# Performance work log

Hardware: AMD Instinct MI355X
Metric: run time of the kernel (lower is better)

The kernel has to match this reference:

```python
import jax, jax.numpy as jnp
import numpy as np

B, BARS, BEATS, FRAC = 64, 16, 4, 8
IN_F = 10 * 47 * 2  # 940
LIN_OUT = 100
BEAT_H = 16
BAR_H = 32


def _p(key, shape, scale=0.05):
    return jax.random.normal(key, shape, dtype=jnp.float32) * scale


def setup_inputs() -> dict:
    key = jax.random.key(0)
    ks = jax.random.split(key, 16)
    return {
        "channels": jax.random.normal(ks[0], (B, BARS, BEATS, FRAC, 10, 2, 47), dtype=jnp.float32),
        "lin_w": _p(ks[1], (LIN_OUT, IN_F)),
        "lin_b": _p(ks[2], (LIN_OUT,)),
        # beats LSTM (unidirectional), PyTorch gate order i,f,g,o
        "b_wih": _p(ks[3], (4 * BEAT_H, LIN_OUT)),
        "b_whh": _p(ks[4], (4 * BEAT_H, BEAT_H)),
        "b_bih": _p(ks[5], (4 * BEAT_H,)),
        "b_bhh": _p(ks[6], (4 * BEAT_H,)),
        # bars LSTM, bidirectional: forward (f_) and reverse (r_) directions
        "f_wih": _p(ks[7], (4 * BAR_H, BEAT_H)),
        "f_whh": _p(ks[8], (4 * BAR_H, BAR_H)),
        "f_bih": _p(ks[9], (4 * BAR_H,)),
        "f_bhh": _p(ks[10], (4 * BAR_H,)),
        "r_wih": _p(ks[11], (4 * BAR_H, BEAT_H)),
        "r_whh": _p(ks[12], (4 * BAR_H, BAR_H)),
        "r_bih": _p(ks[13], (4 * BAR_H,)),
        "r_bhh": _p(ks[14], (4 * BAR_H,)),
    }


def lstm(x, wih, whh, bih, bhh):
    """PyTorch-semantics LSTM, batch_first. x: [N, T, F] -> h_seq [N, T, H]."""
    N = x.shape[0]
    H = whh.shape[1]
    # precompute input contribution for all timesteps
    xg = jnp.einsum('ntf,gf->ntg', x, wih) + (bih + bhh)  # [N, T, 4H]

    def step(carry, xt):
        h, c = carry
        gates = xt + h @ whh.T  # [N, 4H]
        i, f, g, o = jnp.split(gates, 4, axis=-1)
        c = jax.nn.sigmoid(f) * c + jax.nn.sigmoid(i) * jnp.tanh(g)
        h = jax.nn.sigmoid(o) * jnp.tanh(c)
        return (h, c), h

    h0 = jnp.zeros((N, H), x.dtype)
    _, hs = jax.lax.scan(step, (h0, h0), jnp.swapaxes(xg, 0, 1))  # [T, N, H]
    return jnp.swapaxes(hs, 0, 1)


def bilstm(x, f_wih, f_whh, f_bih, f_bhh, r_wih, r_whh, r_bih, r_bhh):
    fwd = lstm(x, f_wih, f_whh, f_bih, f_bhh)
    bwd = jnp.flip(lstm(jnp.flip(x, axis=1), r_wih, r_whh, r_bih, r_bhh), axis=1)
    return jnp.concatenate([fwd, bwd], axis=-1)


def reference(channels, lin_w, lin_b,
              b_wih, b_whh, b_bih, b_bhh,
              f_wih, f_whh, f_bih, f_bhh,
              r_wih, r_whh, r_bih, r_bhh):
    # channels: [B, bars, beats, frac, 10, 2, 47]
    x = jnp.swapaxes(channels, -1, -2)  # [..., 10, 47, 2]
    x = x.reshape(*x.shape[:4], IN_F)   # squash dims 4..6 -> 940
    x = jax.nn.relu(x @ lin_w.T + lin_b)  # [B, bars, beats, frac, 100]

    # Distributed depth=2: fold (B, bars, beats) into batch, seq over frac
    xb = x.reshape(B * BARS * BEATS, FRAC, LIN_OUT)
    beats = lstm(xb, b_wih, b_whh, b_bih, b_bhh)
    beats = beats.reshape(B, BARS, BEATS, FRAC, BEAT_H)

    # last fraction hidden state, then Distributed depth=1 over beats axis
    xl = beats[:, :, :, -1].reshape(B * BARS, BEATS, BEAT_H)
    bars = bilstm(xl, f_wih, f_whh, f_bih, f_bhh, r_wih, r_whh, r_bih, r_bhh)
    bars = bars.reshape(B, BARS, BEATS, 2 * BAR_H)
    return beats, bars
```

## Files before the change

kernel.cpp:

```cpp
#include <hip/hip_runtime.h>
#include <hip/hip_bf16.h>

typedef float f32x4 __attribute__((ext_vector_type(4)));
typedef short bf16x8 __attribute__((ext_vector_type(8)));

#define MFMA16(a, b, c) __builtin_amdgcn_mfma_f32_16x16x32_bf16(a, b, c, 0, 0, 0)

constexpr int K1  = 940;
constexpr int KP2 = 1024;
constexpr int NP  = 112;
constexpr int OSL = 136;

__device__ __forceinline__ float sigf(float x) { return 1.f / (1.f + __expf(-x)); }
__device__ __forceinline__ float tanhfast(float x) { return 2.f / (1.f + __expf(-2.f * x)) - 1.f; }

__device__ __forceinline__ short f2b(float x) {
  __hip_bfloat16 b = __float2bfloat16(x);
  return *reinterpret_cast<short*>(&b);
}

__global__ void prep_kernel(const float* __restrict__ lin_w,
                            const float* __restrict__ b_wih,
                            __hip_bfloat16* __restrict__ w2,
                            __hip_bfloat16* __restrict__ bw2) {
  int idx = blockIdx.x * 256 + threadIdx.x;
  if (idx < NP * KP2) {
    int n = idx >> 10, k = idx & 1023;
    float v = 0.f;
    if (n < 100 && k < K1) {
      int c10 = k / 94, rem = k - c10 * 94;
      int c2 = rem / 47, c47 = rem - c2 * 47;
      int f = c10 * 94 + c47 * 2 + c2;
      v = lin_w[n * K1 + f];
    }
    w2[idx] = __float2bfloat16(v);
  } else {
    int i2 = idx - NP * KP2;
    if (i2 < 64 * 128) {
      int g = i2 >> 7, k = i2 & 127;
      bw2[i2] = __float2bfloat16((k < 100) ? b_wih[g * 100 + k] : 0.f);
    }
  }
}

__global__ __launch_bounds__(256, 2)
void fused_encoder(const float* __restrict__ ch,
                   const __hip_bfloat16* __restrict__ w2,
                   const float* __restrict__ lin_b,
                   const __hip_bfloat16* __restrict__ bw2,
                   const float* __restrict__ bih,
                   const float* __restrict__ bhh,
                   const float* __restrict__ whh,
                   float* __restrict__ beats) {
  __shared__ __align__(16) __hip_bfloat16 out_s[64 * OSL];
  __shared__ float xg_s[64 * 65];

  const int tid = threadIdx.x;
  const int w = tid >> 6, lane = tid & 63;
  const int l16 = lane & 15, bq = lane >> 4;

  const int mbase = blockIdx.x * 64 + w * 16;
  const float* ar = ch + (long)(mbase + l16) * K1 + bq * 8;

  int bidx[7];
#pragma unroll
  for (int nt = 0; nt < 7; ++nt) bidx[nt] = (nt * 16 + l16) * KP2 + bq * 8;

  float lb[7];
#pragma unroll
  for (int nt = 0; nt < 7; ++nt) {
    int col = nt * 16 + l16;
    lb[nt] = (col < 100) ? lin_b[col] : 0.f;
  }

  auto mk = [&](float4 lo, float4 hi) -> bf16x8 {
    return bf16x8{f2b(lo.x), f2b(lo.y), f2b(lo.z), f2b(lo.w),
                  f2b(hi.x), f2b(hi.y), f2b(hi.z), f2b(hi.w)};
  };

  f32x4 acc[7] = {};
  float4 Ab[2][4];
  bf16x8 Bb[2][7];

  const float4 f40{0.f, 0.f, 0.f, 0.f};
  auto ldA = [&](int c, float4* d) {
    const float* p = ar + c * 64;
    if (c < 14) {
      d[0] = *reinterpret_cast<const float4*>(p);
      d[1] = *reinterpret_cast<const float4*>(p + 4);
      d[2] = *reinterpret_cast<const float4*>(p + 32);
      d[3] = *reinterpret_cast<const float4*>(p + 36);
    } else {
      d[0] = *reinterpret_cast<const float4*>(p);
      d[1] = *reinterpret_cast<const float4*>(p + 4);
      d[2] = (bq <= 1) ? *reinterpret_cast<const float4*>(p + 32) : f40;
      d[3] = (bq == 0) ? *reinterpret_cast<const float4*>(p + 36) : f40;
    }
  };
  auto ldB = [&](int ks, bf16x8* d) {
#pragma unroll
    for (int nt = 0; nt < 7; ++nt)
      d[nt] = *reinterpret_cast<const bf16x8*>(&w2[bidx[nt] + ks * 32]);
  };

  ldA(0, Ab[0]);
  ldB(0, Bb[0]);
  ldB(1, Bb[1]);
#pragma unroll
  for (int c = 0; c < 15; ++c) {
    float4* A = Ab[c & 1];
    if (c < 14) ldA(c + 1, Ab[(c + 1) & 1]);
    {
      bf16x8 a = mk(A[0], A[1]);
#pragma unroll
      for (int nt = 0; nt < 7; ++nt) acc[nt] = MFMA16(a, Bb[0][nt], acc[nt]);
    }
    if (c < 14) ldB(2 * c + 2, Bb[0]);
    {
      bf16x8 a = mk(A[2], A[3]);
#pragma unroll
      for (int nt = 0; nt < 7; ++nt) acc[nt] = MFMA16(a, Bb[1][nt], acc[nt]);
    }
    if (c < 14) ldB(2 * c + 3, Bb[1]);
  }

#pragma unroll
  for (int nt = 0; nt < 7; ++nt) {
    const int col = nt * 16 + l16;
#pragma unroll
    for (int r = 0; r < 4; ++r) {
      float v = fmaxf(acc[nt][r] + lb[nt], 0.f);
      out_s[(w * 16 + bq * 4 + r) * OSL + col] = __float2bfloat16((col < 100) ? v : 0.f);
    }
  }
#pragma unroll
  for (int r = 0; r < 4; ++r)
    out_s[(w * 16 + bq * 4 + r) * OSL + 112 + l16] = __float2bfloat16(0.f);

  {
    bf16x8 av[4];
#pragma unroll
    for (int s = 0; s < 4; ++s)
      av[s] = *reinterpret_cast<const bf16x8*>(&out_s[(w * 16 + l16) * OSL + s * 32 + bq * 8]);
    f32x4 xacc[4] = {};
#pragma unroll
    for (int gt = 0; gt < 4; ++gt) {
#pragma unroll
      for (int s = 0; s < 4; ++s) {
        bf16x8 b = *reinterpret_cast<const bf16x8*>(&bw2[(gt * 16 + l16) * 128 + s * 32 + bq * 8]);
        xacc[gt] = MFMA16(av[s], b, xacc[gt]);
      }
    }
#pragma unroll
    for (int gt = 0; gt < 4; ++gt) {
      const int gate = gt * 16 + l16;
      const float bias = bih[gate] + bhh[gate];
#pragma unroll
      for (int r = 0; r < 4; ++r)
        xg_s[(w * 16 + bq * 4 + r) * 65 + gate] = xacc[gt][r] + bias;
    }
  }

  {
    const int cell = lane & 15;
    float wr[16];
#pragma unroll
    for (int u = 0; u < 16; ++u) wr[u] = whh[lane * 16 + u];
    float xv0[8], xv1[8];
#pragma unroll
    for (int t = 0; t < 8; ++t) {
      xv0[t] = xg_s[(w * 16 + t) * 65 + lane];
      xv1[t] = xg_s[(w * 16 + 8 + t) * 65 + lane];
    }
    float h0[16], h1[16];
#pragma unroll
    for (int u = 0; u < 16; ++u) { h0[u] = 0.f; h1[u] = 0.f; }
    float c0 = 0.f, c1 = 0.f;
    const long sg0 = (long)blockIdx.x * 8 + 2 * w;
    const long sg1 = sg0 + 1;
#pragma unroll
    for (int t = 0; t < 8; ++t) {
      float p0 = xv0[t], p1 = xv1[t];
#pragma unroll
      for (int u = 0; u < 16; ++u) { p0 += wr[u] * h0[u]; p1 += wr[u] * h1[u]; }
      const bool istanh = (lane >= 32 && lane < 48);
      float a0 = istanh ? tanhfast(p0) : sigf(p0);
      float a1 = istanh ? tanhfast(p1) : sigf(p1);
      float gi0 = __shfl(a0, cell),      gi1 = __shfl(a1, cell);
      float gf0 = __shfl(a0, cell + 16), gf1 = __shfl(a1, cell + 16);
      float gg0 = __shfl(a0, cell + 32), gg1 = __shfl(a1, cell + 32);
      float go0 = __shfl(a0, cell + 48), go1 = __shfl(a1, cell + 48);
      c0 = gf0 * c0 + gi0 * gg0;
      c1 = gf1 * c1 + gi1 * gg1;
      float hn0 = go0 * tanhfast(c0);
      float hn1 = go1 * tanhfast(c1);
#pragma unroll
      for (int u = 0; u < 16; ++u) { h0[u] = __shfl(hn0, u); h1[u] = __shfl(hn1, u); }
      if (lane < 16) {
        beats[sg0 * 128 + t * 16 + lane] = hn0;
        beats[sg1 * 128 + t * 16 + lane] = hn1;
      }
    }
  }
}

__global__ __launch_bounds__(256)
void bars_bilstm(const float* __restrict__ fwih, const float* __restrict__ fwhh,
                 const float* __restrict__ fbih, const float* __restrict__ fbhh,
                 const float* __restrict__ rwih, const float* __restrict__ rwhh,
                 const float* __restrict__ rbih, const float* __restrict__ rbhh,
                 const float* __restrict__ beats,
                 float* __restrict__ bars) {
  const int tid = threadIdx.x;
  const int dir = tid >> 7, g = tid & 127;
  const int n = blockIdx.x;
  const float* wih = dir ? rwih : fwih;
  const float* whh = dir ? rwhh : fwhh;
  const float bias = dir ? (rbih[g] + rbhh[g]) : (fbih[g] + fbhh[g]);
  float wi[16], wh[32];
#pragma unroll
  for (int u = 0; u < 16; ++u) wi[u] = wih[g * 16 + u];
#pragma unroll
  for (int u = 0; u < 32; ++u) wh[u] = whh[g * 32 + u];
  __shared__ float xbuf[2][16];
  __shared__ float hbuf[2][32];
  __shared__ float gact[2][128];
  float c = 0.f;
  if (g < 32) hbuf[dir][g] = 0.f;
  __syncthreads();
  for (int t = 0; t < 4; ++t) {
    const int tt = dir ? (3 - t) : t;
    if (g < 16) xbuf[dir][g] = beats[((n * 4 + tt) * 8 + 7) * 16 + g];
    __syncthreads();
    float pre = bias;
#pragma unroll
    for (int u = 0; u < 16; ++u) pre += wi[u] * xbuf[dir][u];
#pragma unroll
    for (int u = 0; u < 32; ++u) pre += wh[u] * hbuf[dir][u];
    gact[dir][g] = (g >= 64 && g < 96) ? tanhfast(pre) : sigf(pre);
    __syncthreads();
    if (g < 32) {
      c = gact[dir][32 + g] * c + gact[dir][g] * gact[dir][64 + g];
      float hn = gact[dir][96 + g] * tanhfast(c);
      hbuf[dir][g] = hn;
      bars[(n * 4 + tt) * 64 + dir * 32 + g] = hn;
    }
    __syncthreads();
  }
}

extern "C" void kernel_launch(void* const* d_in, const int* in_sizes, int n_in,
                              void* d_out, int out_size, void* d_ws, size_t ws_size,
                              hipStream_t stream) {
  const float* ch    = (const float*)d_in[0];
  const float* lin_w = (const float*)d_in[1];
  const float* lin_b = (const float*)d_in[2];
  const float* b_wih = (const float*)d_in[3];
  const float* b_whh = (const float*)d_in[4];
  const float* b_bih = (const float*)d_in[5];
  const float* b_bhh = (const float*)d_in[6];
  const float* f_wih = (const float*)d_in[7];
  const float* f_whh = (const float*)d_in[8];
  const float* f_bih = (const float*)d_in[9];
  const float* f_bhh = (const float*)d_in[10];
  const float* r_wih = (const float*)d_in[11];
  const float* r_whh = (const float*)d_in[12];
  const float* r_bih = (const float*)d_in[13];
  const float* r_bhh = (const float*)d_in[14];

  char* ws = (char*)d_ws;
  __hip_bfloat16* w2  = (__hip_bfloat16*)ws;
  __hip_bfloat16* bw2 = (__hip_bfloat16*)(ws + 229376);
  float*          out = (float*)d_out;

  prep_kernel<<<480, 256, 0, stream>>>(lin_w, b_wih, w2, bw2);
  fused_encoder<<<512, 256, 0, stream>>>(ch, w2, lin_b, bw2, b_bih, b_bhh,
                                         b_whh, out);
  bars_bilstm<<<1024, 256, 0, stream>>>(f_wih, f_whh, f_bih, f_bhh,
                                        r_wih, r_whh, r_bih, r_bhh,
                                        out, out + 524288);
}
```

Baseline: 264.9 us.

## Stage linear weight tiles in LDS with double buffering shared across waves

```diff
diff --git a/kernel.cpp b/kernel.cpp
--- a/kernel.cpp
+++ b/kernel.cpp
@@ -10,6 +10,7 @@
 constexpr int KP2 = 1024;
 constexpr int NP  = 112;
 constexpr int OSL = 136;
+constexpr int BSR = 72;
 
 __device__ __forceinline__ float sigf(float x) { return 1.f / (1.f + __expf(-x)); }
 __device__ __forceinline__ float tanhfast(float x) { return 2.f / (1.f + __expf(-2.f * x)) - 1.f; }
@@ -52,8 +53,10 @@
                    const float* __restrict__ bhh,
                    const float* __restrict__ whh,
                    float* __restrict__ beats) {
-  __shared__ __align__(16) __hip_bfloat16 out_s[64 * OSL];
-  __shared__ float xg_s[64 * 65];
+  __shared__ __align__(16) char smem[34048];
+  __hip_bfloat16* Bs    = reinterpret_cast<__hip_bfloat16*>(smem);
+  __hip_bfloat16* out_s = reinterpret_cast<__hip_bfloat16*>(smem);
+  float*          xg_s  = reinterpret_cast<float*>(smem + 17408);
 
   const int tid = threadIdx.x;
   const int w = tid >> 6, lane = tid & 63;
@@ -61,10 +64,6 @@
 
   const int mbase = blockIdx.x * 64 + w * 16;
   const float* ar = ch + (long)(mbase + l16) * K1 + bq * 8;
-
-  int bidx[7];
-#pragma unroll
-  for (int nt = 0; nt < 7; ++nt) bidx[nt] = (nt * 16 + l16) * KP2 + bq * 8;
 
   float lb[7];
 #pragma unroll
@@ -80,7 +79,7 @@
 
   f32x4 acc[7] = {};
   float4 Ab[2][4];
-  bf16x8 Bb[2][7];
+  bf16x8 bst[4];
 
   const float4 f40{0.f, 0.f, 0.f, 0.f};
   auto ldA = [&](int c, float4* d) {
@@ -97,31 +96,50 @@
       d[3] = (bq == 0) ? *reinterpret_cast<const float4*>(p + 36) : f40;
     }
   };
-  auto ldB = [&](int ks, bf16x8* d) {
-#pragma unroll
-    for (int nt = 0; nt < 7; ++nt)
-      d[nt] = *reinterpret_cast<const bf16x8*>(&w2[bidx[nt] + ks * 32]);
+
+  const int sn = tid >> 1, skh = (tid & 1) * 32;
+  auto stageB_ld = [&](int c) {
+    if (sn < NP) {
+      const __hip_bfloat16* src = w2 + sn * KP2 + c * 64 + skh;
+#pragma unroll
+      for (int j = 0; j < 4; ++j)
+        bst[j] = *reinterpret_cast<const bf16x8*>(src + j * 8);
+    }
   };
-
+  auto stageB_st = [&](int buf) {
+    if (sn < NP) {
+      __hip_bfloat16* dst = Bs + buf * (NP * BSR) + sn * BSR + skh;
+#pragma unroll
+      for (int j = 0; j < 4; ++j)
+        *reinterpret_cast<bf16x8*>(dst + j * 8) = bst[j];
+    }
+  };
+
+  stageB_ld(0);
+  stageB_st(0);
   ldA(0, Ab[0]);
-  ldB(0, Bb[0]);
-  ldB(1, Bb[1]);
-#pragma unroll
+  __syncthreads();
+
   for (int c = 0; c < 15; ++c) {
+    if (c < 14) {
+      stageB_ld(c + 1);
+      ldA(c + 1, Ab[(c + 1) & 1]);
+    }
+    const __hip_bfloat16* Bc = Bs + (c & 1) * (NP * BSR);
     float4* A = Ab[c & 1];
-    if (c < 14) ldA(c + 1, Ab[(c + 1) & 1]);
-    {
-      bf16x8 a = mk(A[0], A[1]);
-#pragma unroll
-      for (int nt = 0; nt < 7; ++nt) acc[nt] = MFMA16(a, Bb[0][nt], acc[nt]);
-    }
-    if (c < 14) ldB(2 * c + 2, Bb[0]);
-    {
-      bf16x8 a = mk(A[2], A[3]);
-#pragma unroll
-      for (int nt = 0; nt < 7; ++nt) acc[nt] = MFMA16(a, Bb[1][nt], acc[nt]);
-    }
-    if (c < 14) ldB(2 * c + 3, Bb[1]);
+#pragma unroll
+    for (int ks = 0; ks < 2; ++ks) {
+      bf16x8 bf[7];
+#pragma unroll
+      for (int nt = 0; nt < 7; ++nt)
+        bf[nt] = *reinterpret_cast<const bf16x8*>(
+            &Bc[(nt * 16 + l16) * BSR + ks * 32 + bq * 8]);
+      bf16x8 a = mk(A[2 * ks], A[2 * ks + 1]);
+#pragma unroll
+      for (int nt = 0; nt < 7; ++nt) acc[nt] = MFMA16(a, bf[nt], acc[nt]);
+    }
+    if (c < 14) stageB_st((c + 1) & 1);
+    __syncthreads();
   }
 
 #pragma unroll
```

After: 230.4 us. 1.15x faster.
